# Kernel optimization log

Hardware: AMD Instinct MI355X
Metric: run time of the kernel (lower is better)

## Reference

```python
import jax, jax.numpy as jnp
import numpy as np

N_NODES = 50000
N_EDGES = 640000
D_IN = 128
D_HID = 128
D_OUT = 128


def setup_inputs() -> dict:
    key = jax.random.key(0)
    k1, k2, k3, k4 = jax.random.split(key, 4)
    x = jax.random.normal(k1, (N_NODES, D_IN), dtype=jnp.float32)
    edge_index = jax.random.randint(k2, (2, N_EDGES), 0, N_NODES, dtype=jnp.int32)
    W1 = jax.random.normal(k3, (D_IN, D_HID), dtype=jnp.float32) * (1.0 / np.sqrt(D_IN))
    b1 = jnp.zeros((D_HID,), dtype=jnp.float32)
    W2 = jax.random.normal(k4, (D_HID, D_OUT), dtype=jnp.float32) * (1.0 / np.sqrt(D_HID))
    b2 = jnp.zeros((D_OUT,), dtype=jnp.float32)
    return {"x": x, "edge_index": edge_index, "W1": W1, "b1": b1, "W2": W2, "b2": b2}


def gcn_conv(x, edge_index, W, b, num_nodes):
    # PyG GCNConv: add self-loops, symmetric normalization, linear, aggregate, bias.
    loops = jnp.arange(num_nodes, dtype=edge_index.dtype)
    src = jnp.concatenate([edge_index[0], loops])  # source j
    dst = jnp.concatenate([edge_index[1], loops])  # target i
    deg = jax.ops.segment_sum(jnp.ones_like(dst, dtype=x.dtype), dst,
                              num_segments=num_nodes)  # in-degree incl. self-loop
    dinv = jnp.where(deg > 0, jax.lax.rsqrt(deg), 0.0)
    norm = dinv[src] * dinv[dst]  # [E+N]
    h = x @ W  # [N, hidden]
    msg = norm[:, None] * h[src]  # gather + scale
    out = jax.ops.segment_sum(msg, dst, num_segments=num_nodes)  # scatter-add
    return out + b


def reference(x, edge_index, W1, b1, W2, b2):
    h = gcn_conv(x, edge_index, W1, b1, x.shape[0])
    h = jnp.tanh(h)
    return h @ W2 + b2
```

## Files before the change

### kernel.cpp

```cpp
#include <hip/hip_runtime.h>


#define DFEAT 128
#define CAP 48
#define BROWS 32

typedef __attribute__((ext_vector_type(8))) short short8;
typedef __attribute__((ext_vector_type(4))) float float4v;

__device__ __forceinline__ float bflo(unsigned int u) {
    union { unsigned int i; float f; } v; v.i = u << 16; return v.f;
}
__device__ __forceinline__ float bfhi(unsigned int u) {
    union { unsigned int i; float f; } v; v.i = u & 0xffff0000u; return v.f;
}
__device__ __forceinline__ unsigned short f2bf(float f) {
    union { unsigned int i; float f; } v; v.f = f;
    unsigned int r = v.i + 0x7fffu + ((v.i >> 16) & 1u);
    return (unsigned short)(r >> 16);
}
__device__ __forceinline__ unsigned int pack2(float a, float b) {
    return (unsigned int)f2bf(a) | ((unsigned int)f2bf(b) << 16);
}
__device__ __forceinline__ float fast_tanh(float x) {
    float e = __expf(2.0f * x);
    float r = __builtin_amdgcn_rcpf(e + 1.0f);
    return __builtin_fmaf(-2.0f, r, 1.0f);
}

__global__ void k1_count_fill(const int* __restrict__ dst, int* __restrict__ cnt,
                              int* __restrict__ cnt2, int4* __restrict__ col4,
                              const float* __restrict__ W1, const float* __restrict__ W2,
                              unsigned short* __restrict__ w1f, unsigned short* __restrict__ w2f,
                              int e, int n, int ncol4) {
    int i = blockIdx.x * blockDim.x + threadIdx.x;
    if (i < 2 * DFEAT * DFEAT) {
        int which = i >> 14;
        int idx = i & 16383;
        int k = idx >> 7, nn = idx & 127;
        int f = ((nn >> 4) << 2) + (k >> 5);
        int lane = (nn & 15) | (((k >> 3) & 3) << 4);
        int j = k & 7;
        int o = f * 512 + lane * 8 + j;
        if (which == 0) w1f[o] = f2bf(W1[idx]);
        else            w2f[o] = f2bf(W2[idx]);
    }
    if (i < ncol4) {
        int4 s; s.x = n; s.y = n; s.z = n; s.w = n;
        col4[i] = s;
    }
    if (i < (n + 3) / 4) ((int4*)cnt2)[i] = (int4){0, 0, 0, 0};
    if (i < e) atomicAdd(&cnt[dst[i]], 1);
}

__global__ void k2_scatter_xb(const int* __restrict__ src, const int* __restrict__ dst,
                              const int* __restrict__ cnt, int* __restrict__ cnt2,
                              int* __restrict__ col,
                              const float* __restrict__ x, unsigned int* __restrict__ xb2,
                              int e, int n32) {
    int i = blockIdx.x * blockDim.x + threadIdx.x;
    if (i < n32) {
        float di = rsqrtf((float)(cnt[i >> 5] + 1));
        float4 v = ((const float4*)x)[i];
        xb2[i * 2]     = pack2(v.x * di, v.y * di);
        xb2[i * 2 + 1] = pack2(v.z * di, v.w * di);
    } else if (i < n32 + 32) {
        xb2[i * 2] = 0u;
        xb2[i * 2 + 1] = 0u;
    }
    if (i < e) {
        int d = dst[i];
        int p = atomicAdd(&cnt2[d], 1);
        if (p < CAP) col[d * CAP + p] = src[i];
    }
}

__global__ __launch_bounds__(256) void k_agg_gemm(
    const uint4* __restrict__ xb4, const int* __restrict__ cnt,
    const int* __restrict__ col,
    const unsigned short* __restrict__ w1f, const float* __restrict__ b1,
    const unsigned short* __restrict__ w2f, const float* __restrict__ b2,
    float* __restrict__ out, int n) {
    __shared__ unsigned short aggs[BROWS * 136];
    __shared__ unsigned short hs[BROWS * 136];
    const int t = threadIdx.x;

    const int lane16 = t & 15;
    const int sub = t >> 4;
    for (int g = 0; g < BROWS / 16; ++g) {
        int node_local = g * 16 + sub;
        int node = blockIdx.x * BROWS + node_local;
        int nodec = min(node, n - 1);
        int raw = cnt[nodec];
        int deg = min(raw, CAP);
        float di = rsqrtf((float)(raw + 1));
        uint4 v = xb4[(size_t)nodec * 16 + lane16];
        float a0 = bflo(v.x), a1 = bfhi(v.x), a2 = bflo(v.y), a3 = bfhi(v.y);
        float a4 = bflo(v.z), a5 = bfhi(v.z), a6 = bflo(v.w), a7 = bfhi(v.w);
        const int4* col4 = (const int4*)(col + (size_t)nodec * CAP);
        int nq2 = (deg + 7) >> 3;
        for (int q = 0; q < nq2; ++q) {
            int4 sa = col4[2 * q];
            int4 sb = col4[2 * q + 1];
            uint4 u0 = xb4[(size_t)sa.x * 16 + lane16];
            uint4 u1 = xb4[(size_t)sa.y * 16 + lane16];
            uint4 u2 = xb4[(size_t)sa.z * 16 + lane16];
            uint4 u3 = xb4[(size_t)sa.w * 16 + lane16];
            uint4 u4 = xb4[(size_t)sb.x * 16 + lane16];
            uint4 u5 = xb4[(size_t)sb.y * 16 + lane16];
            uint4 u6 = xb4[(size_t)sb.z * 16 + lane16];
            uint4 u7 = xb4[(size_t)sb.w * 16 + lane16];
            a0 += bflo(u0.x); a1 += bfhi(u0.x); a2 += bflo(u0.y); a3 += bfhi(u0.y);
            a4 += bflo(u0.z); a5 += bfhi(u0.z); a6 += bflo(u0.w); a7 += bfhi(u0.w);
            a0 += bflo(u1.x); a1 += bfhi(u1.x); a2 += bflo(u1.y); a3 += bfhi(u1.y);
            a4 += bflo(u1.z); a5 += bfhi(u1.z); a6 += bflo(u1.w); a7 += bfhi(u1.w);
            a0 += bflo(u2.x); a1 += bfhi(u2.x); a2 += bflo(u2.y); a3 += bfhi(u2.y);
            a4 += bflo(u2.z); a5 += bfhi(u2.z); a6 += bflo(u2.w); a7 += bfhi(u2.w);
            a0 += bflo(u3.x); a1 += bfhi(u3.x); a2 += bflo(u3.y); a3 += bfhi(u3.y);
            a4 += bflo(u3.z); a5 += bfhi(u3.z); a6 += bflo(u3.w); a7 += bfhi(u3.w);
            a0 += bflo(u4.x); a1 += bfhi(u4.x); a2 += bflo(u4.y); a3 += bfhi(u4.y);
            a4 += bflo(u4.z); a5 += bfhi(u4.z); a6 += bflo(u4.w); a7 += bfhi(u4.w);
            a0 += bflo(u5.x); a1 += bfhi(u5.x); a2 += bflo(u5.y); a3 += bfhi(u5.y);
            a4 += bflo(u5.z); a5 += bfhi(u5.z); a6 += bflo(u5.w); a7 += bfhi(u5.w);
            a0 += bflo(u6.x); a1 += bfhi(u6.x); a2 += bflo(u6.y); a3 += bfhi(u6.y);
            a4 += bflo(u6.z); a5 += bfhi(u6.z); a6 += bflo(u6.w); a7 += bfhi(u6.w);
            a0 += bflo(u7.x); a1 += bfhi(u7.x); a2 += bflo(u7.y); a3 += bfhi(u7.y);
            a4 += bflo(u7.z); a5 += bfhi(u7.z); a6 += bflo(u7.w); a7 += bfhi(u7.w);
        }
        uint4 o;
        o.x = pack2(a0 * di, a1 * di);
        o.y = pack2(a2 * di, a3 * di);
        o.z = pack2(a4 * di, a5 * di);
        o.w = pack2(a6 * di, a7 * di);
        *(uint4*)&aggs[node_local * 136 + lane16 * 8] = o;
    }
    __syncthreads();

    const int wave = t >> 6, l = t & 63;
    const int strip = wave >> 1;
    const int colh = wave & 1;
    const int kq = l >> 4;
    const int lc = l & 15;
    const int row_local = strip * 16 + lc;

    float4v acc[4];
    for (int ct = 0; ct < 4; ++ct) acc[ct] = (float4v){0.f, 0.f, 0.f, 0.f};
    for (int kc = 0; kc < 4; ++kc) {
        short8 a = *(const short8*)(aggs + row_local * 136 + kc * 32 + kq * 8);
        for (int ct = 0; ct < 4; ++ct) {
            int ctg = colh * 4 + ct;
            short8 b = *(const short8*)(w1f + (ctg * 4 + kc) * 512 + l * 8);
            acc[ct] = __builtin_amdgcn_mfma_f32_16x16x32_bf16(a, b, acc[ct], 0, 0, 0);
        }
    }
    const int drow0 = strip * 16 + kq * 4;
    for (int ct = 0; ct < 4; ++ct) {
        int c = colh * 64 + ct * 16 + lc;
        float bb = b1[c];
        for (int r = 0; r < 4; ++r) {
            float v = fast_tanh(acc[ct][r] + bb);
            hs[(drow0 + r) * 136 + c] = f2bf(v);
        }
    }
    __syncthreads();

    float4v acc2[4];
    for (int ct = 0; ct < 4; ++ct) acc2[ct] = (float4v){0.f, 0.f, 0.f, 0.f};
    for (int kc = 0; kc < 4; ++kc) {
        short8 a = *(const short8*)(hs + row_local * 136 + kc * 32 + kq * 8);
        for (int ct = 0; ct < 4; ++ct) {
            int ctg = colh * 4 + ct;
            short8 b = *(const short8*)(w2f + (ctg * 4 + kc) * 512 + l * 8);
            acc2[ct] = __builtin_amdgcn_mfma_f32_16x16x32_bf16(a, b, acc2[ct], 0, 0, 0);
        }
    }
    const int orow0 = blockIdx.x * BROWS + drow0;
    for (int ct = 0; ct < 4; ++ct) {
        int c = colh * 64 + ct * 16 + lc;
        float bb = b2[c];
        for (int r = 0; r < 4; ++r) {
            int orow = orow0 + r;
            if (orow < n) out[(size_t)orow * DFEAT + c] = acc2[ct][r] + bb;
        }
    }
}

static inline size_t align256(size_t v) { return (v + 255) & ~(size_t)255; }

extern "C" void kernel_launch(void* const* d_in, const int* in_sizes, int n_in,
                              void* d_out, int out_size, void* d_ws, size_t ws_size,
                              hipStream_t stream) {
    const float* x  = (const float*)d_in[0];
    const int*   ei = (const int*)d_in[1];
    const float* W1 = (const float*)d_in[2];
    const float* b1 = (const float*)d_in[3];
    const float* W2 = (const float*)d_in[4];
    const float* b2 = (const float*)d_in[5];
    float* out = (float*)d_out;

    const int N = in_sizes[0] / DFEAT;
    const int E = in_sizes[1] / 2;
    const int* src = ei;
    const int* dst = ei + E;

    char* ws = (char*)d_ws;
    size_t off = 0;
    int* cnt  = (int*)(ws + off); off += align256((size_t)N * 4);
    int* cnt2 = (int*)(ws + off); off += align256((size_t)N * 4);
    int* col  = (int*)(ws + off); off += align256((size_t)N * CAP * 4);
    unsigned short* xb  = (unsigned short*)(ws + off); off += align256((size_t)(N + 1) * DFEAT * 2);
    unsigned short* w1f = (unsigned short*)(ws + off); off += align256((size_t)DFEAT * DFEAT * 2);
    unsigned short* w2f = (unsigned short*)(ws + off); off += align256((size_t)DFEAT * DFEAT * 2);

    const int ncol4 = N * CAP / 4;
    const int n32 = N * 32;

    int t1 = E > ncol4 ? E : ncol4;
    if (t1 < 2 * DFEAT * DFEAT) t1 = 2 * DFEAT * DFEAT;
    int t2 = (n32 + 32) > E ? (n32 + 32) : E;

    hipMemsetAsync(cnt, 0, (size_t)N * 4, stream);
    k1_count_fill<<<(t1 + 255) / 256, 256, 0, stream>>>(
        dst, cnt, cnt2, (int4*)col, W1, W2, w1f, w2f, E, N, ncol4);
    k2_scatter_xb<<<(t2 + 255) / 256, 256, 0, stream>>>(
        src, dst, cnt, cnt2, col, x, (unsigned int*)xb, E, n32);
    k_agg_gemm<<<(N + BROWS - 1) / BROWS, 256, 0, stream>>>(
        (const uint4*)xb, cnt, col, w1f, b1, w2f, b2, out, N);
}
```

Measured before the change: 195.0 us.

## Build adjacency via partitioned per-block buckets and merge in prep kernel

Replaces the two-pass CSR-like build (count atomics, then a second atomic scatter into a pre-filled capped column array) with a single scatter pass. Edges go into 8 partition-specific buckets chosen by block index, which is meant to reduce atomic contention and remove the second atomic pass. A prep kernel then sums the partition counts to get degrees, merges the buckets into the per-node column list, and pads each list with the sentinel only up to a multiple of 8. This avoids filling the whole column array with sentinels. The cost is a larger workspace, a bigger memset, and a divergent per-node merge loop. Nodes with more than 16 in-edges landing in one partition would be truncated.

```diff
diff --git a/kernel.cpp b/kernel.cpp
--- a/kernel.cpp
+++ b/kernel.cpp
@@ -3,6 +3,8 @@
 
 #define DFEAT 128
 #define CAP 48
+#define CAP8 16
+#define NPART 8
 #define BROWS 32
 
 typedef __attribute__((ext_vector_type(8))) short short8;
@@ -28,11 +30,11 @@
     return __builtin_fmaf(-2.0f, r, 1.0f);
 }
 
-__global__ void k1_count_fill(const int* __restrict__ dst, int* __restrict__ cnt,
-                              int* __restrict__ cnt2, int4* __restrict__ col4,
-                              const float* __restrict__ W1, const float* __restrict__ W2,
-                              unsigned short* __restrict__ w1f, unsigned short* __restrict__ w2f,
-                              int e, int n, int ncol4) {
+__global__ void k_scatter8(const int* __restrict__ src, const int* __restrict__ dst,
+                           int* __restrict__ cnt8, int* __restrict__ col8,
+                           const float* __restrict__ W1, const float* __restrict__ W2,
+                           unsigned short* __restrict__ w1f, unsigned short* __restrict__ w2f,
+                           int e, int n) {
     int i = blockIdx.x * blockDim.x + threadIdx.x;
     if (i < 2 * DFEAT * DFEAT) {
         int which = i >> 14;
@@ -45,33 +47,46 @@
         if (which == 0) w1f[o] = f2bf(W1[idx]);
         else            w2f[o] = f2bf(W2[idx]);
     }
-    if (i < ncol4) {
-        int4 s; s.x = n; s.y = n; s.z = n; s.w = n;
-        col4[i] = s;
-    }
-    if (i < (n + 3) / 4) ((int4*)cnt2)[i] = (int4){0, 0, 0, 0};
-    if (i < e) atomicAdd(&cnt[dst[i]], 1);
-}
-
-__global__ void k2_scatter_xb(const int* __restrict__ src, const int* __restrict__ dst,
-                              const int* __restrict__ cnt, int* __restrict__ cnt2,
-                              int* __restrict__ col,
-                              const float* __restrict__ x, unsigned int* __restrict__ xb2,
-                              int e, int n32) {
+    if (i < e) {
+        int p = blockIdx.x & (NPART - 1);
+        int d = dst[i];
+        int cell = p * n + d;
+        int q = atomicAdd(&cnt8[cell], 1);
+        if (q < CAP8) col8[(size_t)cell * CAP8 + q] = src[i];
+    }
+}
+
+__global__ void k_prep(const float* __restrict__ x, const int* __restrict__ cnt8,
+                       int* __restrict__ cnt, const int* __restrict__ col8,
+                       int* __restrict__ col, unsigned int* __restrict__ xb2, int n) {
     int i = blockIdx.x * blockDim.x + threadIdx.x;
-    if (i < n32) {
-        float di = rsqrtf((float)(cnt[i >> 5] + 1));
+    if (i < n * 32) {
+        int node = i >> 5;
+        int deg = 0;
+        #pragma unroll
+        for (int p = 0; p < NPART; ++p) deg += min(cnt8[p * n + node], CAP8);
+        float di = rsqrtf((float)(deg + 1));
         float4 v = ((const float4*)x)[i];
         xb2[i * 2]     = pack2(v.x * di, v.y * di);
         xb2[i * 2 + 1] = pack2(v.z * di, v.w * di);
-    } else if (i < n32 + 32) {
+    } else if (i < n * 32 + 32) {
         xb2[i * 2] = 0u;
         xb2[i * 2 + 1] = 0u;
     }
-    if (i < e) {
-        int d = dst[i];
-        int p = atomicAdd(&cnt2[d], 1);
-        if (p < CAP) col[d * CAP + p] = src[i];
+    if (i < n) {
+        int k = 0;
+        int* cw = col + (size_t)i * CAP;
+        int total = 0;
+        #pragma unroll
+        for (int p = 0; p < NPART; ++p) {
+            int c = min(cnt8[p * n + i], CAP8);
+            total += c;
+            const int* bp = col8 + (size_t)(p * n + i) * CAP8;
+            for (int j = 0; j < c && k < CAP; ++j) cw[k++] = bp[j];
+        }
+        cnt[i] = total;
+        int kp = (k + 7) & ~7;
+        for (; k < kp; ++k) cw[k] = n;
     }
 }
 
@@ -205,25 +220,22 @@
 
     char* ws = (char*)d_ws;
     size_t off = 0;
+    int* cnt8 = (int*)(ws + off); off += align256((size_t)NPART * N * 4);
     int* cnt  = (int*)(ws + off); off += align256((size_t)N * 4);
-    int* cnt2 = (int*)(ws + off); off += align256((size_t)N * 4);
+    int* col8 = (int*)(ws + off); off += align256((size_t)NPART * N * CAP8 * 4);
     int* col  = (int*)(ws + off); off += align256((size_t)N * CAP * 4);
     unsigned short* xb  = (unsigned short*)(ws + off); off += align256((size_t)(N + 1) * DFEAT * 2);
     unsigned short* w1f = (unsigned short*)(ws + off); off += align256((size_t)DFEAT * DFEAT * 2);
     unsigned short* w2f = (unsigned short*)(ws + off); off += align256((size_t)DFEAT * DFEAT * 2);
 
-    const int ncol4 = N * CAP / 4;
-    const int n32 = N * 32;
-
-    int t1 = E > ncol4 ? E : ncol4;
-    if (t1 < 2 * DFEAT * DFEAT) t1 = 2 * DFEAT * DFEAT;
-    int t2 = (n32 + 32) > E ? (n32 + 32) : E;
-
-    hipMemsetAsync(cnt, 0, (size_t)N * 4, stream);
-    k1_count_fill<<<(t1 + 255) / 256, 256, 0, stream>>>(
-        dst, cnt, cnt2, (int4*)col, W1, W2, w1f, w2f, E, N, ncol4);
-    k2_scatter_xb<<<(t2 + 255) / 256, 256, 0, stream>>>(
-        src, dst, cnt, cnt2, col, x, (unsigned int*)xb, E, n32);
+    int t1 = E > 2 * DFEAT * DFEAT ? E : 2 * DFEAT * DFEAT;
+    int t2 = N * 32 + 32;
+
+    hipMemsetAsync(cnt8, 0, (size_t)NPART * N * 4, stream);
+    k_scatter8<<<(t1 + 255) / 256, 256, 0, stream>>>(
+        src, dst, cnt8, col8, W1, W2, w1f, w2f, E, N);
+    k_prep<<<(t2 + 255) / 256, 256, 0, stream>>>(
+        x, cnt8, cnt, col8, col, (unsigned int*)xb, N);
     k_agg_gemm<<<(N + BROWS - 1) / BROWS, 256, 0, stream>>>(
         (const uint4*)xb, cnt, col, w1f, b1, w2f, b2, out, N);
 }
```

After: 167.9 us. 13.9% less time.
